# Performance work log

Hardware: AMD Instinct MI355X
Metric: run time of the kernel (lower is better)

The kernel has to match this reference:

```python
import jax, jax.numpy as jnp
import numpy as np

N_NODES = 30000
N_REL = 200
N_EDGES = 150000
N_EDGES_NHOP = 30000
NFEAT = 100
NHID = 100
REL_DIM = 100
NHEADS = 2
ALPHA = 0.2  # leaky relu slope


def setup_inputs() -> dict:
    key = jax.random.key(0)
    ks = jax.random.split(key, 16)
    s = 0.1
    D = NHEADS * NHID
    inp = {}
    inp["entity_embeddings"] = jax.random.normal(ks[0], (N_NODES, NFEAT), jnp.float32)
    inp["relation_embed"] = jax.random.normal(ks[1], (N_REL, REL_DIM), jnp.float32)
    inp["edge_list"] = jax.random.randint(ks[2], (2, N_EDGES), 0, N_NODES)
    inp["edge_type"] = jax.random.randint(ks[3], (N_EDGES,), 0, N_REL)
    inp["edge_embed"] = jax.random.normal(ks[4], (N_EDGES, REL_DIM), jnp.float32)
    inp["edge_list_nhop"] = jax.random.randint(ks[5], (2, N_EDGES_NHOP), 0, N_NODES)
    inp["edge_type_nhop"] = jax.random.randint(ks[6], (N_EDGES_NHOP, 2), 0, N_REL)
    inp["entity_embeddings_mapping"] = jax.random.normal(ks[7], (N_NODES, NFEAT), jnp.float32)
    # learned params (xavier-like scale)
    inp["a_heads"] = jax.random.normal(ks[8], (NHEADS, NHID, 2 * NFEAT + REL_DIM), jnp.float32) * s
    inp["a2_heads"] = jax.random.normal(ks[9], (NHEADS, NHID), jnp.float32) * s
    inp["W"] = jax.random.normal(ks[10], (REL_DIM, D), jnp.float32) * s
    inp["a_out"] = jax.random.normal(ks[11], (D, 3 * D), jnp.float32) * s
    inp["a2_out"] = jax.random.normal(ks[12], (D,), jnp.float32) * s
    return inp


def _att_layer(x, src, dst, edge_embed, a, a2, n_nodes, concat):
    # Sparse graph attention (KBGAT style). a: [out, 2*in + rel_dim].
    in_dim = x.shape[1]
    a_src, a_dst, a_rel = a[:, :in_dim], a[:, in_dim:2 * in_dim], a[:, 2 * in_dim:]
    # edge_m = a @ cat(x[src], x[dst], edge_embed)^T, computed without the big concat
    edge_m = x[src] @ a_src.T + x[dst] @ a_dst.T + edge_embed @ a_rel.T  # [E, out]
    powers = -jax.nn.leaky_relu(edge_m @ a2, ALPHA)                      # [E]
    edge_e = jnp.exp(powers)                                             # [E]
    e_rowsum = jax.ops.segment_sum(edge_e, src, num_segments=n_nodes)    # [N]
    e_rowsum = jnp.where(e_rowsum == 0.0, 1e-12, e_rowsum)
    h = jax.ops.segment_sum(edge_e[:, None] * edge_m, src, num_segments=n_nodes)  # [N, out]
    h = h / e_rowsum[:, None]
    return jax.nn.elu(h) if concat else h


def reference(entity_embeddings, relation_embed, edge_list, edge_type, edge_embed,
              edge_list_nhop, edge_type_nhop, entity_embeddings_mapping,
              a_heads, a2_heads, W, a_out, a2_out):
    N = entity_embeddings.shape[0]
    src = jnp.concatenate([edge_list[0], edge_list_nhop[0]])
    dst = jnp.concatenate([edge_list[1], edge_list_nhop[1]])
    # 2-hop edge embedding = sum of the two relation embeddings on the path
    ee_nhop = relation_embed[edge_type_nhop[:, 0]] + relation_embed[edge_type_nhop[:, 1]]
    ee1 = jnp.concatenate([edge_embed, ee_nhop], axis=0)
    h1 = _att_layer(entity_embeddings, src, dst, ee1, a_heads[0], a2_heads[0], N, True)
    h2 = _att_layer(entity_embeddings, src, dst, ee1, a_heads[1], a2_heads[1], N, True)
    h = jnp.concatenate([h1, h2], axis=1)  # [N, 2*nhid]; dropout p=0 (eval)
    out_relation = relation_embed @ W      # [R, 2*nhid]
    ee2 = jnp.concatenate([out_relation[edge_type],
                           out_relation[edge_type_nhop[:, 0]] + out_relation[edge_type_nhop[:, 1]]],
                          axis=0)
    out_entity = _att_layer(h, src, dst, ee2, a_out, a2_out, N, False)
    return jax.nn.elu(out_entity), out_relation
```

## Files before the change

### kernel.cpp

```cpp
#include <hip/hip_runtime.h>

#define N_NODES 30000
#define E1 150000
#define EN 30000
#define ET 180000
#define LALPHA 0.2f
#define NB_SCAN 118

typedef unsigned int u32;
typedef unsigned short u16;
typedef __attribute__((ext_vector_type(8))) short short8;
typedef __attribute__((ext_vector_type(4))) short short4v;
typedef __attribute__((ext_vector_type(4))) float f32x4;

__device__ __forceinline__ float bf2f(u16 u){ return __uint_as_float(((u32)u)<<16); }
__device__ __forceinline__ float2 bfp2(u32 u){
  return make_float2(__uint_as_float(u<<16), __uint_as_float(u & 0xffff0000u));
}
__device__ __forceinline__ u16 f2bf(float f){
  u32 x = __float_as_uint(f);
  return (u16)((x + 0x7fffu + ((x>>16)&1u)) >> 16);
}
__device__ __forceinline__ u32 pk(float x, float y){
  return ((u32)f2bf(x)) | (((u32)f2bf(y))<<16);
}
__device__ __forceinline__ float wredf(float v){
  #pragma unroll
  for(int o=32;o>0;o>>=1) v += __shfl_xor(v, o, 64);
  return v;
}
__device__ __forceinline__ float eluf(float y){ return (y>0.f)? y : expm1f(y); }
__device__ __forceinline__ float ld1(const void* p, int i, int f){
  return f ? ((const float*)p)[i] : bf2f(((const u16*)p)[i]);
}
__device__ __forceinline__ float2 ldp(const void* p, int i, int f){
  if(f){ return ((const float2*)p)[i]; }
  return bfp2(((const u32*)p)[i]);
}
__device__ __forceinline__ void st1(void* p, int i, float v, int f){
  if(f) ((float*)p)[i] = v; else ((u16*)p)[i] = f2bf(v);
}

__device__ __forceinline__ short8 frag_zero(){
  short8 r;
  #pragma unroll
  for(int i=0;i<8;i++) r[i]=0;
  return r;
}
__device__ __forceinline__ short8 ldfragb(const u16* p, int idx){
  short8 r;
  short4v lo = *(const short4v*)(p+idx);
  short4v hi = *(const short4v*)(p+idx+4);
  #pragma unroll
  for(int i=0;i<4;i++){ r[i]=lo[i]; r[4+i]=hi[i]; }
  return r;
}
__device__ __forceinline__ short8 ldfragb16(const u16* p, int idx){
  return *(const short8*)(p+idx);
}
__device__ __forceinline__ short8 ldfragb_p4(const u16* p, int idx){
  short8 r=frag_zero();
  short4v lo = *(const short4v*)(p+idx);
  #pragma unroll
  for(int i=0;i<4;i++) r[i]=lo[i];
  return r;
}
__device__ __forceinline__ short8 ldfrag(const void* p, int idx, int f){
  short8 r;
  if(f){
    const float* fp=(const float*)p+idx;
    #pragma unroll
    for(int i=0;i<8;i++) r[i]=(short)f2bf(fp[i]);
  } else {
    return ldfragb((const u16*)p, idx);
  }
  return r;
}
__device__ __forceinline__ short8 ldfrag_p4(const void* p, int idx, int f){
  short8 r=frag_zero();
  if(f){
    const float* fp=(const float*)p+idx;
    #pragma unroll
    for(int i=0;i<4;i++) r[i]=(short)f2bf(fp[i]);
  } else {
    return ldfragb_p4((const u16*)p, idx);
  }
  return r;
}

__global__ void k_detect(const u32* x, int* flag){
  int t = threadIdx.x;
  int c = 0;
  #pragma unroll
  for(int i=0;i<4;i++){
    u32 v = x[t*4+i];
    u32 lo = v & 0xffffu;
    u32 e = (lo>>7)&0xffu;
    c += (lo==0u || (e>=100u && e<=140u)) ? 1 : 0;
  }
  __shared__ int sd[256];
  sd[t]=c; __syncthreads();
  for(int o=128;o>0;o>>=1){ if(t<o) sd[t]+=sd[t+o]; __syncthreads(); }
  if(t==0) *flag = (sd[0] > 512) ? 0 : 1;
}

__global__ void k_prep(const void* ent, const void* ah, const void* ao, const void* ee,
                       u16* entB, u16* ahB, u16* aoB, u16* eeB, int ws_ok, const int* flag){
  int f = *flag;
  int gid = blockIdx.x*256 + threadIdx.x;
  int stride = gridDim.x*256;
  const int T0=750000, T1=765000, T2=795000, T3=795000+3750000;
  int lim = (f && ws_ok) ? T3 : T2;
  for(int i=gid; i<lim; i+=stride){
    const void* src; u16* dst; int g;
    if(i<T0){ src=ent; dst=entB; g=i; }
    else if(i<T1){ src=ah; dst=ahB; g=i-T0; }
    else if(i<T2){ src=ao; dst=aoB; g=i-T1; }
    else { src=ee; dst=eeB; g=i-T2; }
    if(f){
      float4 v = ((const float4*)src)[g];
      short4v o;
      o[0]=(short)f2bf(v.x); o[1]=(short)f2bf(v.y);
      o[2]=(short)f2bf(v.z); o[3]=(short)f2bf(v.w);
      ((short4v*)dst)[g] = o;
    } else {
      ((short4v*)dst)[g] = ((const short4v*)src)[g];
    }
  }
}

__global__ void k_outrel(const void* rel, const void* W, float* outrel, void* out, const int* flag){
  int f = *flag;
  int t = blockIdx.x*blockDim.x + threadIdx.x;
  if(t >= 200*200) return;
  int r = t / 200, j = t - r*200;
  float acc = 0.f;
  for(int k=0;k<100;k++) acc += ld1(rel, r*100+k, f) * ld1(W, k*200+j, f);
  outrel[t] = acc;
  st1(out, 6000000 + t, acc, f);
}

__global__ void k_small_b(const void* ah, const void* a2h, const void* ao, const void* a2o,
                          float* b1, float* b2, const int* flag){
  int f = *flag;
  int i = blockIdx.x*4 + (threadIdx.x>>6);
  int L = threadIdx.x & 63;
  if(i >= 1200) return;
  float a = 0.f;
  if(i < 600){
    int hd = i/300, k = i - hd*300;
    for(int j=L; j<100; j+=64)
      a += ld1(a2h, hd*100+j, f) * ld1(ah, hd*30000 + j*300 + k, f);
    a = wredf(a);
    if(L==0) b1[i] = a;
  } else {
    int k = i - 600;
    for(int j=L; j<200; j+=64)
      a += ld1(a2o, j, f) * ld1(ao, j*600 + k, f);
    a = wredf(a);
    if(L==0) b2[k] = a;
  }
}

__global__ void k_small_c(const void* rel, const float* outrel, const float* b1, const float* b2,
                          float* c1, float* c2, const int* flag){
  int f = *flag;
  int i = blockIdx.x*4 + (threadIdx.x>>6);
  int L = threadIdx.x & 63;
  if(i >= 600) return;
  float a = 0.f;
  if(i < 400){
    int hd = i/200, r = i - hd*200;
    for(int k=L; k<100; k+=64)
      a += b1[hd*300+200+k] * ld1(rel, r*100+k, f);
    a = wredf(a);
    if(L==0) c1[i] = a;
  } else {
    int r = i - 400;
    for(int k=L; k<200; k+=64)
      a += b2[400+k] * outrel[r*200+k];
    a = wredf(a);
    if(L==0) c2[r] = a;
  }
}

__global__ void k_count(const int* src1, const int* srcN, int* cnt){
  int e = blockIdx.x*256 + threadIdx.x;
  if(e>=ET) return;
  int s = (e<E1)? src1[e] : srcN[e-E1];
  atomicAdd(&cnt[s],1);
}

__global__ void k_scan1(const int* cnt, int* ofs, int* bsum){
  __shared__ int sd[256];
  int b=blockIdx.x, t=threadIdx.x;
  int idx=b*256+t;
  int v=(idx<N_NODES)? cnt[idx] : 0;
  sd[t]=v; __syncthreads();
  for(int o=1;o<256;o<<=1){
    int u=(t>=o)? sd[t-o]:0;
    __syncthreads();
    sd[t]+=u; __syncthreads();
  }
  if(idx<N_NODES) ofs[idx]=sd[t]-v;
  if(t==255) bsum[b]=sd[255];
}

__global__ void k_scan2(const int* bsum, int* bstart, int* ofs){
  __shared__ int sd[128];
  int t=threadIdx.x;
  int v=(t<NB_SCAN)? bsum[t]:0;
  sd[t]=v; __syncthreads();
  for(int o=1;o<128;o<<=1){
    int u=(t>=o)? sd[t-o]:0;
    __syncthreads();
    sd[t]+=u; __syncthreads();
  }
  if(t<NB_SCAN) bstart[t]=sd[t]-v;
  if(t==127) ofs[N_NODES]=sd[127];
}

__global__ void k_scan3(int* ofs, int* cur, const int* bstart){
  int b=blockIdx.x, t=threadIdx.x;
  int idx=b*256+t;
  if(idx>=N_NODES) return;
  int v = ofs[idx] + bstart[b];
  ofs[idx]=v; cur[idx]=v;
}

__global__ void k_scatter(const int* src1, const int* dst1, const int* srcN, const int* dstN,
                          const int* et, const int* etn, int* cur, int* pos, int4* einfo){
  int e = blockIdx.x*256 + threadIdx.x;
  if(e>=ET) return;
  int s,d,t0,t1;
  if(e<E1){ s=src1[e]; d=dst1[e]; t0=et[e]; t1=-1; }
  else { int en=e-E1; s=srcN[en]; d=dstN[en]; t0=etn[en*2]; t1=etn[en*2+1]; }
  int p = atomicAdd(&cur[s],1);
  pos[e]=p;
  einfo[p]=make_int4(e,d,t0,t1);
}

__global__ void k_q1(const u32* entB2, const float* b1, float* q1){
  int n = blockIdx.x*4 + (threadIdx.x>>6);
  if(n>=N_NODES) return;
  int L = threadIdx.x & 63;
  float d00=0,d01=0,d10=0,d11=0;
  if(L<50){
    float2 xv = bfp2(entB2[n*50+L]);
    int k0=2*L;
    d00 = xv.x*b1[k0]     + xv.y*b1[k0+1];
    d01 = xv.x*b1[100+k0] + xv.y*b1[100+k0+1];
    d10 = xv.x*b1[300+k0] + xv.y*b1[300+k0+1];
    d11 = xv.x*b1[400+k0] + xv.y*b1[400+k0+1];
  }
  d00=wredf(d00); d01=wredf(d01); d10=wredf(d10); d11=wredf(d11);
  if(L==0){ q1[n*4+0]=d00; q1[n*4+1]=d01; q1[n*4+2]=d10; q1[n*4+3]=d11; }
}

__global__ __launch_bounds__(256) void k_edge1g(const void* ee, const u16* eeB, int ws_ok,
    const int* src1, const int* dst1, const float* b1, const float* q1,
    const int* pos, float* w1c, const int* flag){
  int f = *flag;
  const void* eeP = (f && ws_ok) ? (const void*)eeB : ee;
  int fe = (f && ws_ok) ? 0 : f;
  int wid = threadIdx.x>>6, l = threadIdx.x&63;
  int lr = l&15, lg = l>>4;
  int m0 = blockIdx.x*128 + wid*32;
  short8 bfr[4];
  #pragma unroll
  for(int ks=0;ks<4;ks++){
    int kb = ks*32 + lg*8;
    short8 b = frag_zero();
    if(lr<2){
      const float* bp = b1 + (lr==0? 200:500);
      #pragma unroll
      for(int i=0;i<8;i++){ int k=kb+i; if(k<100) b[i]=(short)f2bf(bp[k]); }
    }
    bfr[ks]=b;
  }
  int row0 = m0 + lr, row1 = m0 + 16 + lr;
  bool ok0 = row0 < E1, ok1 = row1 < E1;
  f32x4 acc0=(f32x4){0,0,0,0}, acc1=(f32x4){0,0,0,0};
  #pragma unroll
  for(int ks=0;ks<4;ks++){
    int kb = ks*32 + lg*8;
    short8 a0 = frag_zero(), a1 = frag_zero();
    if(ok0){
      if(kb+8<=100) a0 = ldfrag(eeP, row0*100+kb, fe);
      else if(kb<100) a0 = ldfrag_p4(eeP, row0*100+kb, fe);
    }
    if(ok1){
      if(kb+8<=100) a1 = ldfrag(eeP, row1*100+kb, fe);
      else if(kb<100) a1 = ldfrag_p4(eeP, row1*100+kb, fe);
    }
    acc0 = __builtin_amdgcn_mfma_f32_16x16x32_bf16(a0, bfr[ks], acc0, 0,0,0);
    acc1 = __builtin_amdgcn_mfma_f32_16x16x32_bf16(a1, bfr[ks], acc1, 0,0,0);
  }
  if(lr<2){
    #pragma unroll
    for(int mi=0;mi<2;mi++){
      #pragma unroll
      for(int r=0;r<4;r++){
        int e = m0 + mi*16 + lg*4 + r;
        if(e<E1){
          float rv = (mi==0)? acc0[r] : acc1[r];
          int s=src1[e], d=dst1[e];
          float p = q1[s*4+lr*2] + q1[d*4+lr*2+1] + rv;
          p = (p>=0.f)? p : LALPHA*p;
          w1c[2*pos[e] + lr] = expf(-p);
        }
      }
    }
  }
}

__global__ void k_edge1b(const int* etn, const int* srcN, const int* dstN,
                         const float* c1, const float* q1, const int* pos, float* w1c){
  int en = blockIdx.x*256+threadIdx.x;
  if(en>=EN) return;
  int t0=etn[en*2], t1=etn[en*2+1];
  float r0 = c1[t0]+c1[t1];
  float r1 = c1[200+t0]+c1[200+t1];
  int s=srcN[en], d=dstN[en];
  float p0 = q1[s*4+0]+q1[d*4+1]+r0;
  float p1 = q1[s*4+2]+q1[d*4+3]+r1;
  p0=(p0>=0.f)?p0:LALPHA*p0;
  p1=(p1>=0.f)?p1:LALPHA*p1;
  int p = pos[E1+en];
  w1c[2*p]   = expf(-p0);
  w1c[2*p+1] = expf(-p1);
}

__global__ void k_acc1(const int* ofs, const int4* einfo,
                       const u32* entB2, const void* ee, const u32* eeB32, int ws_ok,
                       const void* rel,
                       const float2* w1c, u32* Gq, float* rs1, const int* flag){
  int f = *flag;
  int use_pack = (f==1) && ws_ok;
  int n = blockIdx.x*4 + (threadIdx.x>>6);
  if(n>=N_NODES) return;
  int L = threadIdx.x & 63;
  int beg = ofs[n], end = ofs[n+1];
  float av0x=0,av0y=0,av1x=0,av1y=0, aw0x=0,aw0y=0,aw1x=0,aw1y=0;
  float r0=0, r1=0;
  int i = beg;
  for(; i+3<end; i+=4){
    int4 ei[4]; float2 w[4];
    #pragma unroll
    for(int u=0;u<4;u++) ei[u]=einfo[i+u];
    #pragma unroll
    for(int u=0;u<4;u++) w[u]=w1c[i+u];
    r0 += w[0].x+w[1].x+w[2].x+w[3].x;
    r1 += w[0].y+w[1].y+w[2].y+w[3].y;
    if(L<50){
      float2 xv[4], vv[4];
      #pragma unroll
      for(int u=0;u<4;u++) xv[u]=bfp2(entB2[ei[u].y*50+L]);
      #pragma unroll
      for(int u=0;u<4;u++){
        if(ei[u].w < 0){
          vv[u] = use_pack? bfp2(eeB32[ei[u].x*50+L]) : ldp(ee, ei[u].x*50+L, f);
        } else if(ei[u].x < E1){
          vv[u] = use_pack? bfp2(eeB32[ei[u].x*50+L]) : ldp(ee, ei[u].x*50+L, f);
        } else {
          float2 a=ldp(rel,ei[u].z*50+L,f), b=ldp(rel,ei[u].w*50+L,f);
          vv[u]=make_float2(a.x+b.x, a.y+b.y);
        }
      }
      #pragma unroll
      for(int u=0;u<4;u++){
        av0x += w[u].x*xv[u].x; av0y += w[u].x*xv[u].y;
        av1x += w[u].y*xv[u].x; av1y += w[u].y*xv[u].y;
        aw0x += w[u].x*vv[u].x; aw0y += w[u].x*vv[u].y;
        aw1x += w[u].y*vv[u].x; aw1y += w[u].y*vv[u].y;
      }
    }
  }
  for(; i<end; ++i){
    int4 ei = einfo[i];
    float2 wa = w1c[i];
    r0 += wa.x; r1 += wa.y;
    if(L<50){
      float2 x0 = bfp2(entB2[ei.y*50+L]);
      float2 v0;
      if(ei.x < E1){ v0 = use_pack? bfp2(eeB32[ei.x*50+L]) : ldp(ee, ei.x*50+L, f); }
      else {
        float2 a=ldp(rel,ei.z*50+L,f), b=ldp(rel,ei.w*50+L,f);
        v0=make_float2(a.x+b.x, a.y+b.y);
      }
      av0x += wa.x*x0.x; av0y += wa.x*x0.y;
      av1x += wa.y*x0.x; av1y += wa.y*x0.y;
      aw0x += wa.x*v0.x; aw0y += wa.x*v0.y;
      aw1x += wa.y*v0.x; aw1y += wa.y*v0.y;
    }
  }
  float i0 = (r0==0.f)? 0.f : 1.f/r0;
  float i1 = (r1==0.f)? 0.f : 1.f/r1;
  if(L<50){
    u32* g0 = Gq + n*100;
    u32* g1 = Gq + 3000000 + n*100;
    g0[L]    = pk(av0x*i0, av0y*i0);
    g0[50+L] = pk(aw0x*i0, aw0y*i0);
    g1[L]    = pk(av1x*i1, av1y*i1);
    g1[50+L] = pk(aw1x*i1, aw1y*i1);
  }
  if(L==0){ rs1[n]=r0; rs1[N_NODES+n]=r1; }
}

__global__ __launch_bounds__(256) void k_gemm1m(const u16* G, const u16* ahB, const u16* entB,
                        const float* rs1, u16* Gx2){
  int hd = blockIdx.y;
  int wid = threadIdx.x>>6, l = threadIdx.x&63;
  int lr = l&15, lg = l>>4;
  int m0 = blockIdx.x*32;
  int row0 = m0 + lr, row1 = m0 + 16 + lr;
  bool hi_ok = (m0+16) < N_NODES;
  const u16* Gh0 = G + hd*6000000 + row0*200;
  const u16* Gh1 = G + hd*6000000 + row1*200;
  const u16* A = ahB + hd*30000;
  f32x4 acc[2][2];
  #pragma unroll
  for(int mi=0;mi<2;mi++)
    #pragma unroll
    for(int ntl=0;ntl<2;ntl++) acc[mi][ntl]=(f32x4){0.f,0.f,0.f,0.f};
  #pragma unroll
  for(int k0=0;k0<100;k0+=32){
    int kb = k0 + lg*8;
    short8 a0 = (kb+8<=100)? ldfragb(entB, row0*100+kb)
              : (kb<100    ? ldfragb_p4(entB, row0*100+kb) : frag_zero());
    short8 a1 = frag_zero();
    if(hi_ok){
      if(kb+8<=100) a1 = ldfragb(entB, row1*100+kb);
      else if(kb<100) a1 = ldfragb_p4(entB, row1*100+kb);
    }
    #pragma unroll
    for(int ntl=0;ntl<2;ntl++){
      int j = (ntl*4+wid)*16 + lr;
      short8 b = frag_zero();
      if(j<100){
        if(kb+8<=100) b = ldfragb(A, j*300 + kb);
        else if(kb<100) b = ldfragb_p4(A, j*300 + kb);
      }
      acc[0][ntl] = __builtin_amdgcn_mfma_f32_16x16x32_bf16(a0, b, acc[0][ntl], 0,0,0);
      acc[1][ntl] = __builtin_amdgcn_mfma_f32_16x16x32_bf16(a1, b, acc[1][ntl], 0,0,0);
    }
  }
  #pragma unroll
  for(int k0=0;k0<200;k0+=32){
    int kb = k0 + lg*8;
    short8 a0 = (kb+8<=200)? ldfragb(Gh0, kb) : frag_zero();
    short8 a1 = (hi_ok && kb+8<=200)? ldfragb(Gh1, kb) : frag_zero();
    #pragma unroll
    for(int ntl=0;ntl<2;ntl++){
      int j = (ntl*4+wid)*16 + lr;
      short8 b = (j<100 && kb+8<=200)? ldfragb(A, j*300 + 100 + kb) : frag_zero();
      acc[0][ntl] = __builtin_amdgcn_mfma_f32_16x16x32_bf16(a0, b, acc[0][ntl], 0,0,0);
      acc[1][ntl] = __builtin_amdgcn_mfma_f32_16x16x32_bf16(a1, b, acc[1][ntl], 0,0,0);
    }
  }
  #pragma unroll
  for(int mi=0;mi<2;mi++){
    if(mi==1 && !hi_ok) break;
    #pragma unroll
    for(int r=0;r<4;r++){
      int rr = m0 + mi*16 + lg*4 + r;
      float sc = (rs1[hd*N_NODES+rr]==0.f)? 0.f : 1.f;
      #pragma unroll
      for(int ntl=0;ntl<2;ntl++){
        int j = (ntl*4+wid)*16 + lr;
        if(j<100) Gx2[rr*600 + hd*100 + j] = f2bf(eluf(acc[mi][ntl][r]*sc));
      }
    }
  }
}

__global__ void k_q2(const uint2* hq, const float* b2, float* q2){
  int n = blockIdx.x*4 + (threadIdx.x>>6);
  if(n>=N_NODES) return;
  int L = threadIdx.x&63;
  float ds=0, dd=0;
  if(L<50){
    uint2 hv = hq[n*150+L];
    float2 a = bfp2(hv.x);
    float2 b = bfp2(hv.y);
    int k0=4*L;
    ds = a.x*b2[k0]+a.y*b2[k0+1]+b.x*b2[k0+2]+b.y*b2[k0+3];
    dd = a.x*b2[200+k0]+a.y*b2[200+k0+1]+b.x*b2[200+k0+2]+b.y*b2[200+k0+3];
  }
  ds=wredf(ds); dd=wredf(dd);
  if(L==0){ q2[n*2]=ds; q2[n*2+1]=dd; }
}

__global__ void k_edge2(const int* src1,const int* dst1,const int* srcN,const int* dstN,
                        const int* et, const int* etn, const float* c2, const float* q2,
                        const int* pos, float* w2c){
  int e = blockIdx.x*256+threadIdx.x;
  if(e>=ET) return;
  int s,d; float r;
  if(e<E1){ s=src1[e]; d=dst1[e]; r = c2[et[e]]; }
  else { int en=e-E1; s=srcN[en]; d=dstN[en]; r = c2[etn[en*2]]+c2[etn[en*2+1]]; }
  float p = q2[s*2] + q2[d*2+1] + r;
  p = (p>=0.f)? p : LALPHA*p;
  w2c[pos[e]] = expf(-p);
}

__global__ void k_acc2(const int* ofs, const int4* einfo,
                       u32* Gx2u, const float4* or4, const float* w2c,
                       float* rs2){
  const uint2* h2 = (const uint2*)Gx2u;
  int n = blockIdx.x*4 + (threadIdx.x>>6);
  if(n>=N_NODES) return;
  int L = threadIdx.x&63;
  int beg=ofs[n], end=ofs[n+1];
  float rv=0;
  float avx=0,avy=0,avz=0,avw=0, awx=0,awy=0,awz=0,aww=0;
  int i=beg;
  for(; i+3<end; i+=4){
    int4 ei[4]; float wv[4];
    #pragma unroll
    for(int u=0;u<4;u++) ei[u]=einfo[i+u];
    #pragma unroll
    for(int u=0;u<4;u++) wv[u]=w2c[i+u];
    rv += wv[0]+wv[1]+wv[2]+wv[3];
    if(L<50){
      float2 ha[4], hb[4]; float4 o[4];
      #pragma unroll
      for(int u=0;u<4;u++){ uint2 hv = h2[ei[u].y*150+L]; ha[u]=bfp2(hv.x); hb[u]=bfp2(hv.y); }
      #pragma unroll
      for(int u=0;u<4;u++){
        float4 a = or4[ei[u].z*50+L];
        if(ei[u].w >= 0){
          float4 b = or4[ei[u].w*50+L];
          a = make_float4(a.x+b.x, a.y+b.y, a.z+b.z, a.w+b.w);
        }
        o[u]=a;
      }
      #pragma unroll
      for(int u=0;u<4;u++){
        avx += wv[u]*ha[u].x; avy += wv[u]*ha[u].y;
        avz += wv[u]*hb[u].x; avw += wv[u]*hb[u].y;
        awx += wv[u]*o[u].x;  awy += wv[u]*o[u].y;
        awz += wv[u]*o[u].z;  aww += wv[u]*o[u].w;
      }
    }
  }
  for(; i<end; ++i){
    int4 ei = einfo[i];
    float w0 = w2c[i];
    rv += w0;
    if(L<50){
      uint2 hv = h2[ei.y*150+L];
      float2 ha0=bfp2(hv.x), hb0=bfp2(hv.y);
      float4 o0 = or4[ei.z*50+L];
      if(ei.w >= 0){
        float4 b = or4[ei.w*50+L];
        o0 = make_float4(o0.x+b.x, o0.y+b.y, o0.z+b.z, o0.w+b.w);
      }
      avx += w0*ha0.x; avy += w0*ha0.y; avz += w0*hb0.x; avw += w0*hb0.y;
      awx += w0*o0.x; awy += w0*o0.y; awz += w0*o0.z; aww += w0*o0.w;
    }
  }
  float inv = (rv==0.f)? 0.f : 1.f/rv;
  if(L<50){
    u32* g = Gx2u + n*300 + 100;
    g[2*L]       = pk(avx*inv, avy*inv);
    g[2*L+1]     = pk(avz*inv, avw*inv);
    g[100+2*L]   = pk(awx*inv, awy*inv);
    g[100+2*L+1] = pk(awz*inv, aww*inv);
  }
  if(L==0) rs2[n]=rv;
}

__global__ __launch_bounds__(256) void k_gemm2m(const u16* Gx2, const u16* aoB,
                        const float* rs2, void* out, const int* flag){
  int f = *flag;
  int wid = threadIdx.x>>6, l = threadIdx.x&63;
  int lr = l&15, lg = l>>4;
  int m0 = blockIdx.x*32;
  int row0 = m0 + lr, row1 = m0 + 16 + lr;
  bool hi_ok = (m0+16) < N_NODES;
  const u16* a0p = Gx2 + row0*600;
  const u16* a1p = Gx2 + row1*600;
  f32x4 acc[2][4];
  #pragma unroll
  for(int mi=0;mi<2;mi++)
    #pragma unroll
    for(int ntl=0;ntl<4;ntl++) acc[mi][ntl]=(f32x4){0.f,0.f,0.f,0.f};
  #pragma unroll
  for(int k0=0;k0<600;k0+=32){
    int kb = k0 + lg*8;
    bool kok = (kb+8<=600);
    short8 a0 = kok? ldfragb16(a0p, kb) : frag_zero();
    short8 a1 = (hi_ok && kok)? ldfragb16(a1p, kb) : frag_zero();
    #pragma unroll
    for(int ntl=0;ntl<4;ntl++){
      int j = (ntl*4+wid)*16 + lr;
      short8 b = (j<200 && kok)? ldfragb16(aoB, j*600 + kb) : frag_zero();
      acc[0][ntl] = __builtin_amdgcn_mfma_f32_16x16x32_bf16(a0, b, acc[0][ntl], 0,0,0);
      acc[1][ntl] = __builtin_amdgcn_mfma_f32_16x16x32_bf16(a1, b, acc[1][ntl], 0,0,0);
    }
  }
  #pragma unroll
  for(int mi=0;mi<2;mi++){
    if(mi==1 && !hi_ok) break;
    #pragma unroll
    for(int r=0;r<4;r++){
      int rr = m0 + mi*16 + lg*4 + r;
      float sc = (rs2[rr]==0.f)? 0.f : 1.f;
      #pragma unroll
      for(int ntl=0;ntl<4;ntl++){
        int j = (ntl*4+wid)*16 + lr;
        if(j<200) st1(out, rr*200 + j, eluf(acc[mi][ntl][r]*sc), f);
      }
    }
  }
}

extern "C" void kernel_launch(void* const* d_in, const int* in_sizes, int n_in,
                              void* d_out, int out_size, void* d_ws, size_t ws_size,
                              hipStream_t stream) {
  const void* ent = d_in[0];
  const void* rel = d_in[1];
  const int* el  = (const int*)d_in[2];
  const int* et  = (const int*)d_in[3];
  const void* ee  = d_in[4];
  const int* eln = (const int*)d_in[5];
  const int* etn = (const int*)d_in[6];
  const void* ah  = d_in[8];
  const void* a2h = d_in[9];
  const void* W   = d_in[10];
  const void* ao  = d_in[11];
  const void* a2o = d_in[12];

  float* wsf    = (float*)d_ws;
  int*   flag   = (int*)wsf;
  float* outrel = wsf+4;
  float* b1     = wsf+40008;
  float* b2     = wsf+40608;
  float* c1     = wsf+41208;
  float* c2     = wsf+41608;
  float* q1     = wsf+41808;
  float* q2     = wsf+161808;
  float* w1c    = wsf+221808;
  float* w2c    = wsf+581808;
  float* rs1    = wsf+761808;
  float* rs2    = wsf+821808;
  int*   ofs    = (int*)(wsf+851808);
  int*   cnt    = ofs+30001;
  int*   cur    = cnt+30000;
  int*   bsum   = (int*)(wsf+1121812);
  int*   bstart = bsum+128;
  u16*   G      = (u16*)(wsf+1122072);
  int*   pos    = (int*)(wsf+7122072);
  int4*  einfo  = (int4*)(wsf+7302072);
  u16*   entB   = (u16*)(wsf+10122072);
  u16*   ahB    = (u16*)(wsf+11622072);
  u16*   aoB    = (u16*)(wsf+11652072);
  u16*   eeB    = (u16*)(wsf+11712072);
  u16*   Gx2    = (u16*)(wsf+11712072);
  int ws_ok = (ws_size >= (size_t)19212072*4) ? 1 : 0;

  const int* src1 = el;
  const int* dst1 = el + E1;
  const int* srcN = eln;
  const int* dstN = eln + EN;

  k_detect<<<1,256,0,stream>>>((const u32*)ent, flag);
  hipMemsetAsync(cnt, 0, 30000*sizeof(int), stream);
  k_prep<<<2048,256,0,stream>>>(ent, ah, ao, ee, entB, ahB, aoB, eeB, ws_ok, flag);
  k_small_b<<<300,256,0,stream>>>(ah,a2h,ao,a2o,b1,b2,flag);
  k_outrel<<<(200*200+255)/256,256,0,stream>>>(rel, W, outrel, d_out, flag);
  k_small_c<<<150,256,0,stream>>>(rel, outrel, b1, b2, c1, c2, flag);
  k_count<<<(ET+255)/256,256,0,stream>>>(src1, srcN, cnt);
  k_scan1<<<NB_SCAN,256,0,stream>>>(cnt, ofs, bsum);
  k_scan2<<<1,128,0,stream>>>(bsum, bstart, ofs);
  k_scan3<<<NB_SCAN,256,0,stream>>>(ofs, cur, bstart);
  k_scatter<<<(ET+255)/256,256,0,stream>>>(src1, dst1, srcN, dstN, et, etn, cur, pos, einfo);
  k_q1<<<(N_NODES+3)/4,256,0,stream>>>((const u32*)entB, b1, q1);
  k_edge1g<<<(E1+127)/128,256,0,stream>>>(ee, eeB, ws_ok, src1, dst1, b1, q1, pos, w1c, flag);
  k_edge1b<<<(EN+255)/256,256,0,stream>>>(etn, srcN, dstN, c1, q1, pos, w1c);
  k_acc1<<<(N_NODES+3)/4,256,0,stream>>>(ofs, einfo,
                                         (const u32*)entB, ee, (const u32*)eeB, ws_ok,
                                         rel, (const float2*)w1c, (u32*)G, rs1, flag);
  dim3 g1grid((N_NODES+31)/32, 2);
  k_gemm1m<<<g1grid,256,0,stream>>>(G, ahB, entB, rs1, Gx2);
  k_q2<<<(N_NODES+3)/4,256,0,stream>>>((const uint2*)Gx2, b2, q2);
  k_edge2<<<(ET+255)/256,256,0,stream>>>(src1, dst1, srcN, dstN, et, etn, c2, q2, pos, w2c);
  k_acc2<<<(N_NODES+3)/4,256,0,stream>>>(ofs, einfo,
                                         (u32*)Gx2, (const float4*)outrel, w2c, rs2);
  k_gemm2m<<<(N_NODES+31)/32,256,0,stream>>>(Gx2, aoB, rs2, d_out, flag);
}
```

Measured before the change: 245.0 us.

## Stage A and B tiles in shared memory for second-layer MFMA GEMM

The second-layer GEMM kernel now loads each 32-wide K slice of the activation rows and the full 200-row weight matrix into LDS with cooperative 32-bit loads, then feeds MFMA fragments from LDS instead of issuing strided global fragment loads per wave. This targets redundant global traffic for the shared weight operand across the four waves. It adds two barriers per K step and a full reload of the weight tile per block, which may cost more than it saves. Separately, a redundant branch in the edge aggregation is merged, and the workspace-size threshold for the packed path is raised, which may disable the packed edge-embedding path if the workspace is smaller.

```diff
diff --git a/kernel.cpp b/kernel.cpp
--- a/kernel.cpp
+++ b/kernel.cpp
@@ -358,9 +358,7 @@
       for(int u=0;u<4;u++) xv[u]=bfp2(entB2[ei[u].y*50+L]);
       #pragma unroll
       for(int u=0;u<4;u++){
-        if(ei[u].w < 0){
-          vv[u] = use_pack? bfp2(eeB32[ei[u].x*50+L]) : ldp(ee, ei[u].x*50+L, f);
-        } else if(ei[u].x < E1){
+        if(ei[u].x < E1){
           vv[u] = use_pack? bfp2(eeB32[ei[u].x*50+L]) : ldp(ee, ei[u].x*50+L, f);
         } else {
           float2 a=ldp(rel,ei[u].z*50+L,f), b=ldp(rel,ei[u].w*50+L,f);
@@ -574,31 +572,48 @@
 __global__ __launch_bounds__(256) void k_gemm2m(const u16* Gx2, const u16* aoB,
                         const float* rs2, void* out, const int* flag){
   int f = *flag;
-  int wid = threadIdx.x>>6, l = threadIdx.x&63;
+  __shared__ u16 As[32][36];
+  __shared__ u16 Bs[200][36];
+  int t = threadIdx.x;
+  int wid = t>>6, l = t&63;
   int lr = l&15, lg = l>>4;
   int m0 = blockIdx.x*32;
-  int row0 = m0 + lr, row1 = m0 + 16 + lr;
   bool hi_ok = (m0+16) < N_NODES;
-  const u16* a0p = Gx2 + row0*600;
-  const u16* a1p = Gx2 + row1*600;
   f32x4 acc[2][4];
   #pragma unroll
   for(int mi=0;mi<2;mi++)
     #pragma unroll
     for(int ntl=0;ntl<4;ntl++) acc[mi][ntl]=(f32x4){0.f,0.f,0.f,0.f};
-  #pragma unroll
   for(int k0=0;k0<600;k0+=32){
-    int kb = k0 + lg*8;
-    bool kok = (kb+8<=600);
-    short8 a0 = kok? ldfragb16(a0p, kb) : frag_zero();
-    short8 a1 = (hi_ok && kok)? ldfragb16(a1p, kb) : frag_zero();
+    int klen = (600-k0>=32)? 32 : (600-k0);
+    int words = klen>>1;
+    for(int idx=t; idx<32*words; idx+=256){
+      int r = idx/words, w = idx - r*words;
+      int rr = m0 + r; if(rr >= N_NODES) rr = N_NODES-1;
+      u32 v = *(const u32*)(Gx2 + rr*600 + k0 + 2*w);
+      *(u32*)&As[r][2*w] = v;
+    }
+    for(int idx=t; idx<200*words; idx+=256){
+      int r = idx/words, w = idx - r*words;
+      u32 v = *(const u32*)(aoB + r*600 + k0 + 2*w);
+      *(u32*)&Bs[r][2*w] = v;
+    }
+    __syncthreads();
+    int kb = lg*8;
+    bool kok = (kb+8<=klen);
+    short8 a0 = frag_zero(), a1 = frag_zero();
+    if(kok){
+      a0 = ldfragb(&As[lr][0], kb);
+      a1 = ldfragb(&As[16+lr][0], kb);
+    }
     #pragma unroll
     for(int ntl=0;ntl<4;ntl++){
       int j = (ntl*4+wid)*16 + lr;
-      short8 b = (j<200 && kok)? ldfragb16(aoB, j*600 + kb) : frag_zero();
+      short8 b = (j<200 && kok)? ldfragb(&Bs[0][0], j*36 + kb) : frag_zero();
       acc[0][ntl] = __builtin_amdgcn_mfma_f32_16x16x32_bf16(a0, b, acc[0][ntl], 0,0,0);
       acc[1][ntl] = __builtin_amdgcn_mfma_f32_16x16x32_bf16(a1, b, acc[1][ntl], 0,0,0);
     }
+    __syncthreads();
   }
   #pragma unroll
   for(int mi=0;mi<2;mi++){
@@ -658,7 +673,7 @@
   u16*   aoB    = (u16*)(wsf+11652072);
   u16*   eeB    = (u16*)(wsf+11712072);
   u16*   Gx2    = (u16*)(wsf+11712072);
-  int ws_ok = (ws_size >= (size_t)19212072*4) ? 1 : 0;
+  int ws_ok = (ws_size >= (size_t)20712072*4) ? 1 : 0;
 
   const int* src1 = el;
   const int* dst1 = el + E1;
```

Result: slower. 279.4 us (+14.0%).
